# Optimization experiments

Hardware: AMD Instinct MI355X
Metric: run time of the kernel (lower is better)

Reference implementation:

```python
import jax, jax.numpy as jnp
import numpy as np
from jax import lax

C1 = (0.01 * 255.0) ** 2
C2 = (0.03 * 255.0) ** 2
_Y_WEIGHTS = np.array([65.738, 129.057, 25.064], dtype=np.float32) / 256.0


def _box11(x):
    # 11x11 uniform box filter, padding=5, NCHW single-channel
    k = jnp.ones((1, 1, 11, 11), x.dtype) / 121.0
    return lax.conv_general_dilated(
        x, k, window_strides=(1, 1), padding=[(5, 5), (5, 5)],
        dimension_numbers=("NCHW", "OIHW", "NCHW"))


def setup_inputs() -> dict:
    key = jax.random.key(0)
    k1, k2 = jax.random.split(key)
    sr = jax.random.uniform(k1, (16, 3, 512, 512), dtype=jnp.float32) * 255.0
    hr = jax.random.uniform(k2, (16, 3, 512, 512), dtype=jnp.float32) * 255.0
    return {"sr": sr, "hr": hr, "batch_size": 16}


def reference(sr, hr, batch_size):
    rgb_range = 255.0
    scale = 4
    sr = jnp.clip(sr / rgb_range, 0.0, 1.0)
    hr = jnp.clip(hr / rgb_range, 0.0, 1.0)
    shave = scale + 6  # = 10; W=512 > 2*shave, so full shave branch
    sr = sr[..., shave:-shave, shave:-shave]
    hr = hr[..., shave:-shave, shave:-shave]
    # RGB -> Y (C > 1)
    w = jnp.asarray(_Y_WEIGHTS, sr.dtype).reshape(1, 3, 1, 1)
    sr = jnp.sum(sr * w, axis=1, keepdims=True)  # [B,1,h,w]
    hr = jnp.sum(hr * w, axis=1, keepdims=True)
    mu1 = _box11(sr)
    mu2 = _box11(hr)
    mu1_sq = mu1 * mu1
    mu2_sq = mu2 * mu2
    mu1_mu2 = mu1 * mu2
    sigma1_sq = _box11(sr * sr) - mu1_sq
    sigma2_sq = _box11(hr * hr) - mu2_sq
    sigma12 = _box11(sr * hr) - mu1_mu2
    ssim_map = ((2.0 * mu1_mu2 + C1) * (2.0 * sigma12 + C2)) / (
        (mu1_sq + mu2_sq + C1) * (sigma1_sq + sigma2_sq + C2))
    return jnp.sum(1.0 - ssim_map) / batch_size
```

## Files before the change

### kernel.cpp

```cpp
#include <hip/hip_runtime.h>


#define IMG    512
#define SHAVE  10
#define OUTW   492
#define TILE   32
#define HALO   5
#define REG    (TILE + 2*HALO)
#define NTILES 16
#define NBATCH 16

__global__ __launch_bounds__(256)
void ssim_tile_kernel(const float* __restrict__ sr,
                      const float* __restrict__ hr,
                      double* __restrict__ acc)
{
    __shared__ float ys[REG][REG];
    __shared__ float yh[REG][REG];
    __shared__ float hsS [REG][TILE];
    __shared__ float hsH [REG][TILE];
    __shared__ float hsSS[REG][TILE];
    __shared__ float hsHH[REG][TILE];
    __shared__ float hsSH[REG][TILE];
    __shared__ float wpart[4];

    const int b   = blockIdx.z;
    const int oy0 = blockIdx.y * TILE;
    const int ox0 = blockIdx.x * TILE;
    const int tid = threadIdx.x;

    const float inv255 = 1.0f / 255.0f;
    const float w0 = 65.738f  / 256.0f;
    const float w1 = 129.057f / 256.0f;
    const float w2 = 25.064f  / 256.0f;

    const size_t cstride = (size_t)IMG * IMG;
    const size_t base    = (size_t)b * 3 * cstride;

    for (int i = tid; i < REG * REG; i += 256) {
        const int r  = i / REG;
        const int c  = i - r * REG;
        const int sy = oy0 - HALO + r;
        const int sx = ox0 - HALO + c;
        const size_t idx = base + (size_t)(sy + SHAVE) * IMG + (sx + SHAVE);
        float vs = 0.0f, vh = 0.0f;
        if (sy >= 0 && sy < OUTW && sx >= 0 && sx < OUTW) {
            float s0 = fminf(fmaxf(sr[idx]               * inv255, 0.0f), 1.0f);
            float s1 = fminf(fmaxf(sr[idx +     cstride] * inv255, 0.0f), 1.0f);
            float s2 = fminf(fmaxf(sr[idx + 2 * cstride] * inv255, 0.0f), 1.0f);
            float h0 = fminf(fmaxf(hr[idx]               * inv255, 0.0f), 1.0f);
            float h1 = fminf(fmaxf(hr[idx +     cstride] * inv255, 0.0f), 1.0f);
            float h2 = fminf(fmaxf(hr[idx + 2 * cstride] * inv255, 0.0f), 1.0f);
            vs = w0 * s0 + w1 * s1 + w2 * s2;
            vh = w0 * h0 + w1 * h1 + w2 * h2;
        }
        ys[r][c] = vs;
        yh[r][c] = vh;
    }
    __syncthreads();

    for (int i = tid; i < REG * TILE; i += 256) {
        const int r = i >> 5;
        const int c = i & (TILE - 1);
        float s = 0.f, h = 0.f, ss = 0.f, hh = 0.f, sh = 0.f;
#pragma unroll
        for (int dx = 0; dx < 11; ++dx) {
            const float a = ys[r][c + dx];
            const float g = yh[r][c + dx];
            s  += a;     h  += g;
            ss += a * a; hh += g * g; sh += a * g;
        }
        hsS [r][c] = s;  hsH [r][c] = h;
        hsSS[r][c] = ss; hsHH[r][c] = hh; hsSH[r][c] = sh;
    }
    __syncthreads();

    const float C1 = 6.5025f;
    const float C2 = 58.5225f;
    const float inv121 = 1.0f / 121.0f;
    float local = 0.0f;
    for (int p = tid; p < TILE * TILE; p += 256) {
        const int oyl = p >> 5;
        const int oxl = p & (TILE - 1);
        const int oy  = oy0 + oyl;
        const int ox  = ox0 + oxl;
        if (oy < OUTW && ox < OUTW) {
            float s = 0.f, h = 0.f, ss = 0.f, hh = 0.f, sh = 0.f;
#pragma unroll
            for (int dy = 0; dy < 11; ++dy) {
                s  += hsS [oyl + dy][oxl];
                h  += hsH [oyl + dy][oxl];
                ss += hsSS[oyl + dy][oxl];
                hh += hsHH[oyl + dy][oxl];
                sh += hsSH[oyl + dy][oxl];
            }
            const float mu1   = s * inv121;
            const float mu2   = h * inv121;
            const float mu1sq = mu1 * mu1;
            const float mu2sq = mu2 * mu2;
            const float mu12  = mu1 * mu2;
            const float sig1  = ss * inv121 - mu1sq;
            const float sig2  = hh * inv121 - mu2sq;
            const float sig12 = sh * inv121 - mu12;
            const float num = (2.0f * mu12 + C1) * (2.0f * sig12 + C2);
            const float den = (mu1sq + mu2sq + C1) * (sig1 + sig2 + C2);
            local += 1.0f - num / den;
        }
    }

#pragma unroll
    for (int off = 32; off > 0; off >>= 1)
        local += __shfl_down(local, off, 64);
    const int lane = tid & 63;
    const int wv   = tid >> 6;
    if (lane == 0) wpart[wv] = local;
    __syncthreads();
    if (tid == 0) {
        const float tot = wpart[0] + wpart[1] + wpart[2] + wpart[3];
        atomicAdd(acc, (double)tot);
    }
}

__global__ void ssim_finalize(const double* __restrict__ acc,
                              float* __restrict__ out)
{
    out[0] = (float)(acc[0] / (double)NBATCH);
}

extern "C" void kernel_launch(void* const* d_in, const int* in_sizes, int n_in,
                              void* d_out, int out_size, void* d_ws, size_t ws_size,
                              hipStream_t stream)
{
    const float* sr = (const float*)d_in[0];
    const float* hr = (const float*)d_in[1];
    double* acc = (double*)d_ws;
    float* out  = (float*)d_out;

    hipMemsetAsync(d_ws, 0, sizeof(double), stream);

    dim3 grid(NTILES, NTILES, NBATCH);
    ssim_tile_kernel<<<grid, 256, 0, stream>>>(sr, hr, acc);
    ssim_finalize<<<1, 1, 0, stream>>>(acc, out);
}
```

Baseline: 171.2 us.

## Replace two-pass shared box filter with register sliding window and partial sums

Drops the intermediate horizontal-sum shared arrays. Each thread now owns one column and four output rows, computes the horizontal sums directly from interleaved float2 luma in shared memory, and keeps a running vertical sum in registers. The global double atomic and the memset are replaced by per-block partials that a 256-thread finalize kernel reduces. This removes one barrier and most shared-memory traffic and raises occupancy, but threads now redo horizontal sums for overlapping rows, and per-block partials need workspace sized for all blocks.

```diff
diff --git a/kernel.cpp b/kernel.cpp
--- a/kernel.cpp
+++ b/kernel.cpp
@@ -9,25 +9,39 @@
 #define REG    (TILE + 2*HALO)
 #define NTILES 16
 #define NBATCH 16
+#define NBLOCKS (NTILES*NTILES*NBATCH)
 
-__global__ __launch_bounds__(256)
+__device__ __forceinline__ float ssim_term(float s, float h, float ss, float hh, float sh)
+{
+    const float C1 = 6.5025f;
+    const float C2 = 58.5225f;
+    const float inv121 = 1.0f / 121.0f;
+    const float mu1   = s * inv121;
+    const float mu2   = h * inv121;
+    const float mu1sq = mu1 * mu1;
+    const float mu2sq = mu2 * mu2;
+    const float mu12  = mu1 * mu2;
+    const float sig1  = ss * inv121 - mu1sq;
+    const float sig2  = hh * inv121 - mu2sq;
+    const float sig12 = sh * inv121 - mu12;
+    const float num = (2.0f * mu12 + C1) * (2.0f * sig12 + C2);
+    const float den = (mu1sq + mu2sq + C1) * (sig1 + sig2 + C2);
+    return 1.0f - num / den;
+}
+
+__global__ __launch_bounds__(256, 4)
 void ssim_tile_kernel(const float* __restrict__ sr,
                       const float* __restrict__ hr,
-                      double* __restrict__ acc)
+                      double* __restrict__ partials)
 {
-    __shared__ float ys[REG][REG];
-    __shared__ float yh[REG][REG];
-    __shared__ float hsS [REG][TILE];
-    __shared__ float hsH [REG][TILE];
-    __shared__ float hsSS[REG][TILE];
-    __shared__ float hsHH[REG][TILE];
-    __shared__ float hsSH[REG][TILE];
-    __shared__ float wpart[4];
+    __shared__ float2 y2[REG][REG];
+    __shared__ double wsum[4];
 
     const int b   = blockIdx.z;
     const int oy0 = blockIdx.y * TILE;
     const int ox0 = blockIdx.x * TILE;
     const int tid = threadIdx.x;
+    const int bid = blockIdx.x + NTILES * (blockIdx.y + NTILES * blockIdx.z);
 
     const float inv255 = 1.0f / 255.0f;
     const float w0 = 65.738f  / 256.0f;
@@ -42,9 +56,9 @@
         const int c  = i - r * REG;
         const int sy = oy0 - HALO + r;
         const int sx = ox0 - HALO + c;
-        const size_t idx = base + (size_t)(sy + SHAVE) * IMG + (sx + SHAVE);
         float vs = 0.0f, vh = 0.0f;
         if (sy >= 0 && sy < OUTW && sx >= 0 && sx < OUTW) {
+            const size_t idx = base + (size_t)(sy + SHAVE) * IMG + (sx + SHAVE);
             float s0 = fminf(fmaxf(sr[idx]               * inv255, 0.0f), 1.0f);
             float s1 = fminf(fmaxf(sr[idx +     cstride] * inv255, 0.0f), 1.0f);
             float s2 = fminf(fmaxf(sr[idx + 2 * cstride] * inv255, 0.0f), 1.0f);
@@ -54,58 +68,51 @@
             vs = w0 * s0 + w1 * s1 + w2 * s2;
             vh = w0 * h0 + w1 * h1 + w2 * h2;
         }
-        ys[r][c] = vs;
-        yh[r][c] = vh;
+        y2[r][c] = make_float2(vs, vh);
     }
     __syncthreads();
 
-    for (int i = tid; i < REG * TILE; i += 256) {
-        const int r = i >> 5;
-        const int c = i & (TILE - 1);
+    const int oxl = tid & 31;
+    const int grp = tid >> 5;
+    const int u0  = grp * 4;
+    const int ox  = ox0 + oxl;
+
+    float rS = 0.f, rH = 0.f, rSS = 0.f, rHH = 0.f, rSH = 0.f;
+    float tS[3], tH[3], tSS[3], tHH[3], tSH[3];
+
+    double local = 0.0;
+
+#pragma unroll
+    for (int u = 0; u < 11; ++u) {
         float s = 0.f, h = 0.f, ss = 0.f, hh = 0.f, sh = 0.f;
 #pragma unroll
-        for (int dx = 0; dx < 11; ++dx) {
-            const float a = ys[r][c + dx];
-            const float g = yh[r][c + dx];
-            s  += a;     h  += g;
-            ss += a * a; hh += g * g; sh += a * g;
+        for (int j = 0; j < 11; ++j) {
+            const float2 v = y2[u0 + u][oxl + j];
+            s  += v.x;       h  += v.y;
+            ss += v.x * v.x; hh += v.y * v.y; sh += v.x * v.y;
         }
-        hsS [r][c] = s;  hsH [r][c] = h;
-        hsSS[r][c] = ss; hsHH[r][c] = hh; hsSH[r][c] = sh;
+        rS += s; rH += h; rSS += ss; rHH += hh; rSH += sh;
+        if (u < 3) { tS[u] = s; tH[u] = h; tSS[u] = ss; tHH[u] = hh; tSH[u] = sh; }
     }
-    __syncthreads();
+    if (ox < OUTW && (oy0 + u0) < OUTW)
+        local += (double)ssim_term(rS, rH, rSS, rHH, rSH);
 
-    const float C1 = 6.5025f;
-    const float C2 = 58.5225f;
-    const float inv121 = 1.0f / 121.0f;
-    float local = 0.0f;
-    for (int p = tid; p < TILE * TILE; p += 256) {
-        const int oyl = p >> 5;
-        const int oxl = p & (TILE - 1);
-        const int oy  = oy0 + oyl;
-        const int ox  = ox0 + oxl;
-        if (oy < OUTW && ox < OUTW) {
-            float s = 0.f, h = 0.f, ss = 0.f, hh = 0.f, sh = 0.f;
 #pragma unroll
-            for (int dy = 0; dy < 11; ++dy) {
-                s  += hsS [oyl + dy][oxl];
-                h  += hsH [oyl + dy][oxl];
-                ss += hsSS[oyl + dy][oxl];
-                hh += hsHH[oyl + dy][oxl];
-                sh += hsSH[oyl + dy][oxl];
-            }
-            const float mu1   = s * inv121;
-            const float mu2   = h * inv121;
-            const float mu1sq = mu1 * mu1;
-            const float mu2sq = mu2 * mu2;
-            const float mu12  = mu1 * mu2;
-            const float sig1  = ss * inv121 - mu1sq;
-            const float sig2  = hh * inv121 - mu2sq;
-            const float sig12 = sh * inv121 - mu12;
-            const float num = (2.0f * mu12 + C1) * (2.0f * sig12 + C2);
-            const float den = (mu1sq + mu2sq + C1) * (sig1 + sig2 + C2);
-            local += 1.0f - num / den;
+    for (int k = 1; k <= 3; ++k) {
+        float s = 0.f, h = 0.f, ss = 0.f, hh = 0.f, sh = 0.f;
+#pragma unroll
+        for (int j = 0; j < 11; ++j) {
+            const float2 v = y2[u0 + 10 + k][oxl + j];
+            s  += v.x;       h  += v.y;
+            ss += v.x * v.x; hh += v.y * v.y; sh += v.x * v.y;
         }
+        rS  += s  - tS [k - 1];
+        rH  += h  - tH [k - 1];
+        rSS += ss - tSS[k - 1];
+        rHH += hh - tHH[k - 1];
+        rSH += sh - tSH[k - 1];
+        if (ox < OUTW && (oy0 + u0 + k) < OUTW)
+            local += (double)ssim_term(rS, rH, rSS, rHH, rSH);
     }
 
 #pragma unroll
@@ -113,18 +120,31 @@
         local += __shfl_down(local, off, 64);
     const int lane = tid & 63;
     const int wv   = tid >> 6;
-    if (lane == 0) wpart[wv] = local;
+    if (lane == 0) wsum[wv] = local;
     __syncthreads();
-    if (tid == 0) {
-        const float tot = wpart[0] + wpart[1] + wpart[2] + wpart[3];
-        atomicAdd(acc, (double)tot);
-    }
+    if (tid == 0)
+        partials[bid] = wsum[0] + wsum[1] + wsum[2] + wsum[3];
 }
 
-__global__ void ssim_finalize(const double* __restrict__ acc,
-                              float* __restrict__ out)
+__global__ __launch_bounds__(256)
+void ssim_finalize(const double* __restrict__ partials,
+                   float* __restrict__ out)
 {
-    out[0] = (float)(acc[0] / (double)NBATCH);
+    __shared__ double wsum[4];
+    const int tid = threadIdx.x;
+    double local = 0.0;
+#pragma unroll
+    for (int i = 0; i < NBLOCKS / 256; ++i)
+        local += partials[tid + 256 * i];
+#pragma unroll
+    for (int off = 32; off > 0; off >>= 1)
+        local += __shfl_down(local, off, 64);
+    const int lane = tid & 63;
+    const int wv   = tid >> 6;
+    if (lane == 0) wsum[wv] = local;
+    __syncthreads();
+    if (tid == 0)
+        out[0] = (float)((wsum[0] + wsum[1] + wsum[2] + wsum[3]) / (double)NBATCH);
 }
 
 extern "C" void kernel_launch(void* const* d_in, const int* in_sizes, int n_in,
@@ -133,12 +153,10 @@
 {
     const float* sr = (const float*)d_in[0];
     const float* hr = (const float*)d_in[1];
-    double* acc = (double*)d_ws;
-    float* out  = (float*)d_out;
-
-    hipMemsetAsync(d_ws, 0, sizeof(double), stream);
+    double* partials = (double*)d_ws;
+    float* out = (float*)d_out;
 
     dim3 grid(NTILES, NTILES, NBATCH);
-    ssim_tile_kernel<<<grid, 256, 0, stream>>>(sr, hr, acc);
-    ssim_finalize<<<1, 1, 0, stream>>>(acc, out);
+    ssim_tile_kernel<<<grid, 256, 0, stream>>>(sr, hr, partials);
+    ssim_finalize<<<1, 256, 0, stream>>>(partials, out);
 }
```

After: 629.9 us. +268.0%, slower.
